# Performance work log

Measured on AMD Instinct MI355X. Metric: run time of the kernel, lower is better.

## Reference

```python
import jax, jax.numpy as jnp
import numpy as np

B, T, C = 4, 2048, 2048
H = 16
D = C // H  # head_dim = 128
THETA = 10000.0


def rope_cos_sin(t, d, dtype=jnp.float32):
    inv_freq = 1.0 / (THETA ** (jnp.arange(0, d, 2, dtype=jnp.float32) / d))  # [D/2]
    pos = jnp.arange(t, dtype=jnp.float32)
    freqs = jnp.outer(pos, inv_freq)                 # [T, D/2]
    emb = jnp.concatenate([freqs, freqs], axis=-1)   # [T, D]
    return jnp.cos(emb).astype(dtype), jnp.sin(emb).astype(dtype)


def rotate_half(x):
    x1, x2 = jnp.split(x, 2, axis=-1)
    return jnp.concatenate([-x2, x1], axis=-1)


def setup_inputs() -> dict:
    key = jax.random.key(0)
    k1, k2, k3 = jax.random.split(key, 3)
    x = jax.random.normal(k1, (B, T, C), dtype=jnp.float32)
    Wqkv = jax.random.normal(k2, (C, 3 * C), dtype=jnp.float32) * (1.0 / np.sqrt(C))
    Wout = jax.random.normal(k3, (C, C), dtype=jnp.float32) * (1.0 / np.sqrt(C))
    return {"x": x, "Wqkv": Wqkv, "Wout": Wout}


def reference(x, Wqkv, Wout):
    b, t, c = x.shape
    qkv = jnp.einsum('btc,cd->btd', x, Wqkv)          # [B,T,3C]
    q, k, v = jnp.split(qkv, 3, axis=-1)
    # [B,T,C] -> [B,H,T,D]
    q = q.reshape(b, t, H, D).transpose(0, 2, 1, 3)
    k = k.reshape(b, t, H, D).transpose(0, 2, 1, 3)
    v = v.reshape(b, t, H, D).transpose(0, 2, 1, 3)
    cos, sin = rope_cos_sin(t, D, x.dtype)            # [T,D]
    cos = cos[None, None]                             # [1,1,T,D]
    sin = sin[None, None]
    q = q * cos + rotate_half(q) * sin
    k = k * cos + rotate_half(k) * sin
    scale = 1.0 / np.sqrt(D)
    scores = jnp.einsum('bhqd,bhkd->bhqk', q, k) * scale
    causal = jnp.tril(jnp.ones((t, t), dtype=bool))
    scores = jnp.where(causal[None, None], scores, jnp.finfo(scores.dtype).min)
    attn = jax.nn.softmax(scores, axis=-1)
    y = jnp.einsum('bhqk,bhkd->bhqd', attn, v)        # [B,H,T,D]
    y = y.transpose(0, 2, 1, 3).reshape(b, t, c)      # [B,T,C]
    return jnp.einsum('btc,cd->btd', y, Wout)
```

## Files before the change

kernel.cpp:

```cpp
#include <hip/hip_runtime.h>
#include <hip/hip_bf16.h>
#include <cmath>

#define Bsz   4
#define Tlen  2048
#define Cdim  2048
#define Hn    16
#define Dh    128
#define N_QKV 6144
#define Mrows 8192

typedef __bf16 bf16x8 __attribute__((ext_vector_type(8)));
typedef __bf16 bf16x4 __attribute__((ext_vector_type(4)));
typedef float  f32x4  __attribute__((ext_vector_type(4)));

__device__ __forceinline__ f32x4 mfma16(bf16x8 a, bf16x8 b, f32x4 c) {
  return __builtin_amdgcn_mfma_f32_16x16x32_bf16(a, b, c, 0, 0, 0);
}

__device__ __forceinline__ void gl16(const void* g, void* l) {
  __builtin_amdgcn_global_load_lds(
      (const __attribute__((address_space(1))) void*)g,
      (__attribute__((address_space(3))) void*)l, 16, 0, 0);
}

__global__ void rope_table_k(float* __restrict__ cosT, float* __restrict__ sinT) {
  int idx = blockIdx.x * 256 + threadIdx.x;
  int t = idx >> 6, i = idx & 63;
  float invf = __expf(-(float)i * 0.14391156698f);
  float a = (float)t * invf;
  float s, c;
  sincosf(a, &s, &c);
  cosT[idx] = c;
  sinT[idx] = s;
}

__global__ __launch_bounds__(256) void f32_to_bf16_k(
    const float* __restrict__ src, __bf16* __restrict__ dst) {
  size_t i = ((size_t)blockIdx.x * 256 + threadIdx.x) * 8;
  f32x4 a = *(const f32x4*)(src + i);
  f32x4 b = *(const f32x4*)(src + i + 4);
  bf16x8 o;
  o[0] = (__bf16)a[0]; o[1] = (__bf16)a[1]; o[2] = (__bf16)a[2]; o[3] = (__bf16)a[3];
  o[4] = (__bf16)b[0]; o[5] = (__bf16)b[1]; o[6] = (__bf16)b[2]; o[7] = (__bf16)b[3];
  *(bf16x8*)(dst + i) = o;
}

__global__ __launch_bounds__(256) void transpose_to_bf16_k(
    const float* __restrict__ src, __bf16* __restrict__ dst, int K, int N) {
  __shared__ float tile[32][33];
  int n0 = blockIdx.x * 32, k0 = blockIdx.y * 32;
  int tr = threadIdx.x >> 3, tc = (threadIdx.x & 7) * 4;
  f32x4 v = *(const f32x4*)&src[(size_t)(k0 + tr) * N + n0 + tc];
  tile[tr][tc + 0] = v[0]; tile[tr][tc + 1] = v[1];
  tile[tr][tc + 2] = v[2]; tile[tr][tc + 3] = v[3];
  __syncthreads();
  bf16x4 w;
  w[0] = (__bf16)tile[tc + 0][tr];
  w[1] = (__bf16)tile[tc + 1][tr];
  w[2] = (__bf16)tile[tc + 2][tr];
  w[3] = (__bf16)tile[tc + 3][tr];
  *(bf16x4*)&dst[(size_t)(n0 + tr) * K + k0 + tc] = w;
}

__global__ __launch_bounds__(512, 2) void qkv_gemm(
    const __bf16* __restrict__ Xb, const __bf16* __restrict__ Wt,
    __bf16* __restrict__ Qo, __bf16* __restrict__ Ko, __bf16* __restrict__ Vo,
    const float* __restrict__ cosT, const float* __restrict__ sinT)
{
  __shared__ union SM {
    struct { __bf16 A[2][256 * 64]; __bf16 B[2][256 * 64]; } s;
    float C[64][265];
  } sm;

  const int tid = threadIdx.x, lane = tid & 63, wid = tid >> 6;
  const int g = lane >> 4, l16 = lane & 15;
  const int wr = wid >> 2, wc = wid & 3;

  const int bid = blockIdx.x;
  const int xcd = bid & 7, idx = bid >> 3;
  const int stl = idx >> 4, pos = idx & 15;
  const int m0 = (xcd * 4 + (pos >> 2)) * 256;
  const int n0 = (stl * 4 + (pos & 3)) * 256;

  const int srow = tid >> 3;
  const int schk = (tid & 7) ^ (srow & 7);
  const __bf16* gA = Xb + (size_t)(m0 + srow) * Cdim + schk * 8;
  const __bf16* gB = Wt + (size_t)(n0 + srow) * Cdim + schk * 8;
  const int ldst = wid * 512;

  f32x4 acc[8][4] = {};
  const int NT = Cdim / 64;

  #pragma unroll
  for (int r = 0; r < 4; ++r) {
    gl16(gA + (size_t)r * 64 * Cdim, &sm.s.A[0][r * 4096 + ldst]);
    gl16(gB + (size_t)r * 64 * Cdim, &sm.s.B[0][r * 4096 + ldst]);
  }
  #pragma unroll
  for (int r = 0; r < 4; ++r) {
    gl16(gA + 64 + (size_t)r * 64 * Cdim, &sm.s.A[1][r * 4096 + ldst]);
    gl16(gB + 64 + (size_t)r * 64 * Cdim, &sm.s.B[1][r * 4096 + ldst]);
  }

  for (int t = 0; t < NT; ++t) {
    const int p = t & 1;
    if (t < NT - 1) asm volatile("s_waitcnt vmcnt(8)" ::: "memory");
    else            asm volatile("s_waitcnt vmcnt(0)" ::: "memory");
    __builtin_amdgcn_s_barrier();
    __builtin_amdgcn_sched_barrier(0);

    #pragma unroll
    for (int kk = 0; kk < 2; ++kk) {
      bf16x8 a[8], b[4];
      const int ch = (((kk << 2) | g) ^ (l16 & 7)) * 8;
      #pragma unroll
      for (int f = 0; f < 8; ++f)
        a[f] = *(const bf16x8*)&sm.s.A[p][(wr * 128 + f * 16 + l16) * 64 + ch];
      #pragma unroll
      for (int n = 0; n < 4; ++n)
        b[n] = *(const bf16x8*)&sm.s.B[p][(wc * 64 + n * 16 + l16) * 64 + ch];
      #pragma unroll
      for (int f = 0; f < 8; ++f)
        #pragma unroll
        for (int n = 0; n < 4; ++n)
          acc[f][n] = mfma16(a[f], b[n], acc[f][n]);
    }

    __builtin_amdgcn_sched_barrier(0);
    asm volatile("s_waitcnt lgkmcnt(0)" ::: "memory");
    __builtin_amdgcn_s_barrier();

    if (t + 2 < NT) {
      const __bf16* pA = gA + (size_t)(t + 2) * 64;
      const __bf16* pB = gB + (size_t)(t + 2) * 64;
      #pragma unroll
      for (int r = 0; r < 4; ++r) {
        gl16(pA + (size_t)r * 64 * Cdim, &sm.s.A[p][r * 4096 + ldst]);
        gl16(pB + (size_t)r * 64 * Cdim, &sm.s.B[p][r * 4096 + ldst]);
      }
    }
  }

  const int sel = n0 >> 11;
  const int h0  = (n0 & 2047) >> 7;
  const int erow = tid >> 3, q = tid & 7;
  const int dlo = (q & 3) * 16;
  const int clo = (q >> 2) * 128 + dlo;
  const int vcol = tid >> 1, vth = tid & 1;

  #pragma unroll
  for (int rh = 0; rh < 4; ++rh) {
    if (wr == (rh >> 1)) {
      const int fb = (rh & 1) * 4;
      #pragma unroll
      for (int f2 = 0; f2 < 4; ++f2)
        #pragma unroll
        for (int n = 0; n < 4; ++n)
          #pragma unroll
          for (int r = 0; r < 4; ++r)
            sm.C[f2 * 16 + g * 4 + r][wc * 64 + n * 16 + l16] = acc[fb + f2][n][r];
    }
    __syncthreads();
    if (sel == 2) {
      const int hh = h0 + (vcol >> 7), d = vcol & 127;
      const int mb = m0 + rh * 64 + vth * 32;
      const int b_ = mb >> 11, tt = mb & 2047;
      __bf16* outp = Vo + (((size_t)(b_ * Hn + hh)) * Dh + d) * Tlen + tt;
      bf16x8 w[4];
      #pragma unroll
      for (int i = 0; i < 32; ++i)
        w[i >> 3][i & 7] = (__bf16)sm.C[vth * 32 + i][vcol];
      #pragma unroll
      for (int k = 0; k < 4; ++k) *(bf16x8*)&outp[k * 8] = w[k];
    } else {
      __bf16* dst = (sel == 0) ? Qo : Ko;
      const int m = m0 + rh * 64 + erow;
      const int b_ = m >> 11, t = m & 2047;
      __bf16* out = dst + (((size_t)(b_ * Hn + h0 + (q >> 2))) * Tlen + t) * Dh + dlo;
      const float* cb = cosT + t * 64 + dlo;
      const float* sb = sinT + t * 64 + dlo;
      bf16x8 o1[2], o2[2];
      #pragma unroll
      for (int i = 0; i < 16; ++i) {
        float v1 = sm.C[erow][clo + i];
        float v2 = sm.C[erow][clo + i + 64];
        float cs = cb[i], sn = sb[i];
        float r1 = v1 * cs - v2 * sn;
        float r2 = v2 * cs + v1 * sn;
        o1[i >> 3][i & 7] = (__bf16)r1;
        o2[i >> 3][i & 7] = (__bf16)r2;
      }
      *(bf16x8*)&out[0]  = o1[0];
      *(bf16x8*)&out[8]  = o1[1];
      *(bf16x8*)&out[64] = o2[0];
      *(bf16x8*)&out[72] = o2[1];
    }
    __syncthreads();
  }
}

__global__ __launch_bounds__(256, 2) void attn_fwd(
    const __bf16* __restrict__ Qg, const __bf16* __restrict__ Kg,
    const __bf16* __restrict__ Vtg, __bf16* __restrict__ Yg)
{
  __shared__ __bf16 Ks[2][64 * 128];
  __shared__ __bf16 Vt[2][128 * 64];
  __shared__ __bf16 Ps[4][16][72];

  const int tid = threadIdx.x, lane = tid & 63, wid = tid >> 6;
  const int g = lane >> 4, l16 = lane & 15;
  const int qt = gridDim.x - 1 - blockIdx.x;
  const int q0 = qt * 64;
  const size_t bh = (size_t)blockIdx.z * Hn + blockIdx.y;
  const __bf16* Kbase = Kg + bh * ((size_t)Tlen * Dh);
  const __bf16* Vbase = Vtg + bh * ((size_t)Dh * Tlen);

  bf16x8 aq[4];
  {
    const __bf16* qrow = Qg + (bh * Tlen + q0 + wid * 16 + l16) * Dh;
    #pragma unroll
    for (int ks = 0; ks < 4; ++ks)
      aq[ks] = *(const bf16x8*)(qrow + ks * 32 + 8 * g);
  }

  float m_r[4], l_r[4];
  #pragma unroll
  for (int r = 0; r < 4; ++r) { m_r[r] = -1e30f; l_r[r] = 0.f; }
  f32x4 o[8] = {};

  const int NKV = qt + 1;

  const int krow = lane >> 4, kchk = lane & 15;
  const int vrow = lane >> 3, vchk = lane & 7;

#define STAGE_KV(kv0_, buf_)                                                    \
  {                                                                             \
    _Pragma("unroll")                                                           \
    for (int rr = 0; rr < 4; ++rr) {                                            \
      const int row = wid * 16 + rr * 4 + krow;                                 \
      const int sc = kchk ^ (row & 7);                                          \
      gl16(Kbase + (size_t)((kv0_) + row) * Dh + sc * 8,                        \
           &Ks[buf_][(wid * 16 + rr * 4) * 128]);                               \
    }                                                                           \
    _Pragma("unroll")                                                           \
    for (int rr = 0; rr < 4; ++rr) {                                            \
      const int row = wid * 32 + rr * 8 + vrow;                                 \
      const int sc = vchk ^ (row & 7);                                          \
      gl16(Vbase + (size_t)row * Tlen + (kv0_) + sc * 8,                        \
           &Vt[buf_][(wid * 32 + rr * 8) * 64]);                                \
    }                                                                           \
  }

  STAGE_KV(0, 0);

  for (int it = 0; it < NKV; ++it) {
    const int p = it & 1;
    if (it + 1 < NKV) {
      STAGE_KV((it + 1) * 64, (it + 1) & 1);
      asm volatile("s_waitcnt vmcnt(8)" ::: "memory");
    } else {
      asm volatile("s_waitcnt vmcnt(0)" ::: "memory");
    }
    __builtin_amdgcn_s_barrier();
    __builtin_amdgcn_sched_barrier(0);

    f32x4 s[4] = {};
    #pragma unroll
    for (int ks = 0; ks < 4; ++ks) {
      const int ch = ((4 * ks + g) ^ (l16 & 7)) * 8;
      #pragma unroll
      for (int nf = 0; nf < 4; ++nf) {
        bf16x8 bk = *(const bf16x8*)&Ks[p][(nf * 16 + l16) * 128 + ch];
        s[nf] = mfma16(aq[ks], bk, s[nf]);
      }
    }

    const float scl = 0.08838834764831845f;
    #pragma unroll
    for (int nf = 0; nf < 4; ++nf)
      #pragma unroll
      for (int r = 0; r < 4; ++r) s[nf][r] *= scl;
    if ((it + 1) * 64 > q0) {
      #pragma unroll
      for (int nf = 0; nf < 4; ++nf) {
        const int col = nf * 16 + l16;
        #pragma unroll
        for (int r = 0; r < 4; ++r)
          if (col > wid * 16 + 4 * g + r) s[nf][r] = -1e30f;
      }
    }

    float mx[4];
    #pragma unroll
    for (int r = 0; r < 4; ++r)
      mx[r] = fmaxf(fmaxf(s[0][r], s[1][r]), fmaxf(s[2][r], s[3][r]));
    #pragma unroll
    for (int off = 1; off < 16; off <<= 1)
      #pragma unroll
      for (int r = 0; r < 4; ++r)
        mx[r] = fmaxf(mx[r], __shfl_xor(mx[r], off, 64));

    int grow = 0;
    #pragma unroll
    for (int r = 0; r < 4; ++r) grow |= (mx[r] > m_r[r]) ? 1 : 0;
    if (__any(grow)) {
      #pragma unroll
      for (int r = 0; r < 4; ++r) {
        const float mn = fmaxf(m_r[r], mx[r]);
        const float al = __expf(m_r[r] - mn);
        m_r[r] = mn;
        l_r[r] *= al;
        #pragma unroll
        for (int n2 = 0; n2 < 8; ++n2) o[n2][r] *= al;
      }
    }

    float rs[4] = {0.f, 0.f, 0.f, 0.f};
    #pragma unroll
    for (int nf = 0; nf < 4; ++nf)
      #pragma unroll
      for (int r = 0; r < 4; ++r) {
        const float pv = __expf(s[nf][r] - m_r[r]);
        s[nf][r] = pv;
        rs[r] += pv;
      }
    #pragma unroll
    for (int off = 1; off < 16; off <<= 1)
      #pragma unroll
      for (int r = 0; r < 4; ++r) rs[r] += __shfl_xor(rs[r], off, 64);
    #pragma unroll
    for (int r = 0; r < 4; ++r) l_r[r] += rs[r];

    #pragma unroll
    for (int nf = 0; nf < 4; ++nf)
      #pragma unroll
      for (int r = 0; r < 4; ++r)
        Ps[wid][4 * g + r][nf * 16 + l16] = (__bf16)s[nf][r];
    asm volatile("s_waitcnt lgkmcnt(0)" ::: "memory");
    __builtin_amdgcn_sched_barrier(0);

    bf16x8 pa0 = *(const bf16x8*)&Ps[wid][l16][8 * g];
    bf16x8 pa1 = *(const bf16x8*)&Ps[wid][l16][32 + 8 * g];
    const int c0 = (g ^ (l16 & 7)) * 8;
    const int c1 = ((4 + g) ^ (l16 & 7)) * 8;
    #pragma unroll
    for (int n2 = 0; n2 < 8; ++n2) {
      bf16x8 vb0 = *(const bf16x8*)&Vt[p][(n2 * 16 + l16) * 64 + c0];
      bf16x8 vb1 = *(const bf16x8*)&Vt[p][(n2 * 16 + l16) * 64 + c1];
      o[n2] = mfma16(pa0, vb0, o[n2]);
      o[n2] = mfma16(pa1, vb1, o[n2]);
    }

    asm volatile("s_waitcnt lgkmcnt(0)" ::: "memory");
    __builtin_amdgcn_sched_barrier(0);
    __builtin_amdgcn_s_barrier();
  }
#undef STAGE_KV

  float inv[4];
  #pragma unroll
  for (int r = 0; r < 4; ++r) inv[r] = 1.0f / l_r[r];
  __bf16* ybase = Yg + ((size_t)(blockIdx.z * Tlen + q0 + wid * 16)) * Cdim
                + blockIdx.y * Dh;
  #pragma unroll
  for (int n2 = 0; n2 < 8; ++n2)
    #pragma unroll
    for (int r = 0; r < 4; ++r)
      ybase[(size_t)(4 * g + r) * Cdim + n2 * 16 + l16] = (__bf16)(o[n2][r] * inv[r]);
}

__global__ __launch_bounds__(512, 2) void out_gemm(
    const __bf16* __restrict__ Yb, const __bf16* __restrict__ Wt,
    float* __restrict__ O)
{
  __shared__ struct { __bf16 A[2][256 * 64]; __bf16 B[2][256 * 64]; } sm;

  const int tid = threadIdx.x, lane = tid & 63, wid = tid >> 6;
  const int g = lane >> 4, l16 = lane & 15;
  const int wr = wid >> 2, wc = wid & 3;

  const int bid = blockIdx.x;
  const int xcd = bid & 7, idx = bid >> 3;
  const int stl = idx >> 4, pos = idx & 15;
  const int m0 = (xcd * 4 + (pos >> 2)) * 256;
  const int n0 = (stl * 4 + (pos & 3)) * 256;

  const int srow = tid >> 3;
  const int schk = (tid & 7) ^ (srow & 7);
  const __bf16* gA = Yb + (size_t)(m0 + srow) * Cdim + schk * 8;
  const __bf16* gB = Wt + (size_t)(n0 + srow) * Cdim + schk * 8;
  const int ldst = wid * 512;

  f32x4 acc[8][4] = {};
  const int NT = Cdim / 64;

  #pragma unroll
  for (int r = 0; r < 4; ++r) {
    gl16(gA + (size_t)r * 64 * Cdim, &sm.A[0][r * 4096 + ldst]);
    gl16(gB + (size_t)r * 64 * Cdim, &sm.B[0][r * 4096 + ldst]);
  }
  #pragma unroll
  for (int r = 0; r < 4; ++r) {
    gl16(gA + 64 + (size_t)r * 64 * Cdim, &sm.A[1][r * 4096 + ldst]);
    gl16(gB + 64 + (size_t)r * 64 * Cdim, &sm.B[1][r * 4096 + ldst]);
  }

  for (int t = 0; t < NT; ++t) {
    const int p = t & 1;
    if (t < NT - 1) asm volatile("s_waitcnt vmcnt(8)" ::: "memory");
    else            asm volatile("s_waitcnt vmcnt(0)" ::: "memory");
    __builtin_amdgcn_s_barrier();
    __builtin_amdgcn_sched_barrier(0);

    #pragma unroll
    for (int kk = 0; kk < 2; ++kk) {
      bf16x8 a[8], b[4];
      const int ch = (((kk << 2) | g) ^ (l16 & 7)) * 8;
      #pragma unroll
      for (int f = 0; f < 8; ++f)
        a[f] = *(const bf16x8*)&sm.A[p][(wr * 128 + f * 16 + l16) * 64 + ch];
      #pragma unroll
      for (int n = 0; n < 4; ++n)
        b[n] = *(const bf16x8*)&sm.B[p][(wc * 64 + n * 16 + l16) * 64 + ch];
      #pragma unroll
      for (int f = 0; f < 8; ++f)
        #pragma unroll
        for (int n = 0; n < 4; ++n)
          acc[f][n] = mfma16(a[f], b[n], acc[f][n]);
    }

    __builtin_amdgcn_sched_barrier(0);
    asm volatile("s_waitcnt lgkmcnt(0)" ::: "memory");
    __builtin_amdgcn_s_barrier();

    if (t + 2 < NT) {
      const __bf16* pA = gA + (size_t)(t + 2) * 64;
      const __bf16* pB = gB + (size_t)(t + 2) * 64;
      #pragma unroll
      for (int r = 0; r < 4; ++r) {
        gl16(pA + (size_t)r * 64 * Cdim, &sm.A[p][r * 4096 + ldst]);
        gl16(pB + (size_t)r * 64 * Cdim, &sm.B[p][r * 4096 + ldst]);
      }
    }
  }

  #pragma unroll
  for (int f = 0; f < 8; ++f)
    #pragma unroll
    for (int n = 0; n < 4; ++n)
      #pragma unroll
      for (int r = 0; r < 4; ++r)
        O[(size_t)(m0 + wr * 128 + f * 16 + g * 4 + r) * Cdim
          + (n0 + wc * 64 + n * 16 + l16)] = acc[f][n][r];
}

extern "C" void kernel_launch(void* const* d_in, const int* in_sizes, int n_in,
                              void* d_out, int out_size, void* d_ws, size_t ws_size,
                              hipStream_t stream) {
  const float* x    = (const float*)d_in[0];
  const float* Wqkv = (const float*)d_in[1];
  const float* Wout = (const float*)d_in[2];
  float* out = (float*)d_out;

  float*  cosT   = (float*)d_ws;
  float*  sinT   = cosT + Tlen * 64;
  __bf16* Xb     = (__bf16*)(sinT + Tlen * 64);
  __bf16* Wqkv_t = Xb + (size_t)Mrows * Cdim;
  __bf16* Wout_t = Wqkv_t + (size_t)N_QKV * Cdim;
  __bf16* Qb     = Wout_t + (size_t)Cdim * Cdim;
  __bf16* Kb     = Qb + (size_t)Bsz * Hn * Tlen * Dh;
  __bf16* Vb     = Kb + (size_t)Bsz * Hn * Tlen * Dh;
  __bf16* Yb     = Xb;

  rope_table_k<<<dim3(512), dim3(256), 0, stream>>>(cosT, sinT);
  f32_to_bf16_k<<<dim3(Mrows * Cdim / (256 * 8)), dim3(256), 0, stream>>>(x, Xb);
  transpose_to_bf16_k<<<dim3(N_QKV / 32, Cdim / 32), dim3(256), 0, stream>>>(
      Wqkv, Wqkv_t, Cdim, N_QKV);
  transpose_to_bf16_k<<<dim3(Cdim / 32, Cdim / 32), dim3(256), 0, stream>>>(
      Wout, Wout_t, Cdim, Cdim);
  qkv_gemm<<<dim3(768), dim3(512), 0, stream>>>(
      Xb, Wqkv_t, Qb, Kb, Vb, cosT, sinT);
  attn_fwd<<<dim3(Tlen / 64, Hn, Bsz), dim3(256), 0, stream>>>(Qb, Kb, Vb, Yb);
  out_gemm<<<dim3(256), dim3(512), 0, stream>>>(Yb, Wout_t, out);
}
```

Before: 732.2 us.

## Transpose attention MFMA operands so each lane owns one query row

Swaps the MFMA operand order in both attention matmuls so the accumulator is transposed and each lane holds a single query row. The row max and row sum then need two cross-lane shuffles instead of four-step reductions over four rows. The softmax folds scale and log2e into an exp2 FMA, applies the causal mask only on the diagonal tile, packs P into 32-bit LDS words, and writes the output as vectorized bf16x4 stores. It also raises wave priority around the MFMA loops with s_setprio. This trades the VALU and shuffle overhead of softmax for new LDS index patterns that could add bank conflicts.

```diff
diff --git a/kernel.cpp b/kernel.cpp
--- a/kernel.cpp
+++ b/kernel.cpp
@@ -13,6 +13,7 @@
 typedef __bf16 bf16x8 __attribute__((ext_vector_type(8)));
 typedef __bf16 bf16x4 __attribute__((ext_vector_type(4)));
 typedef float  f32x4  __attribute__((ext_vector_type(4)));
+typedef uint32_t u32x2 __attribute__((ext_vector_type(2)));
 
 __device__ __forceinline__ f32x4 mfma16(bf16x8 a, bf16x8 b, f32x4 c) {
   return __builtin_amdgcn_mfma_f32_16x16x32_bf16(a, b, c, 0, 0, 0);
@@ -22,6 +23,12 @@
   __builtin_amdgcn_global_load_lds(
       (const __attribute__((address_space(1))) void*)g,
       (__attribute__((address_space(3))) void*)l, 16, 0, 0);
+}
+
+__device__ __forceinline__ uint32_t pack_bf16(float lo, float hi) {
+  union { __bf16 h; unsigned short u; } a, b;
+  a.h = (__bf16)lo; b.h = (__bf16)hi;
+  return (uint32_t)a.u | ((uint32_t)b.u << 16);
 }
 
 __global__ void rope_table_k(float* __restrict__ cosT, float* __restrict__ sinT) {
@@ -206,7 +213,7 @@
 {
   __shared__ __bf16 Ks[2][64 * 128];
   __shared__ __bf16 Vt[2][128 * 64];
-  __shared__ __bf16 Ps[4][16][72];
+  __shared__ uint32_t Ps2[4][16 * 34 + 2];
 
   const int tid = threadIdx.x, lane = tid & 63, wid = tid >> 6;
   const int g = lane >> 4, l16 = lane & 15;
@@ -216,18 +223,19 @@
   const __bf16* Kbase = Kg + bh * ((size_t)Tlen * Dh);
   const __bf16* Vbase = Vtg + bh * ((size_t)Dh * Tlen);
 
+  const int q_glob = q0 + wid * 16 + l16;
+
   bf16x8 aq[4];
   {
-    const __bf16* qrow = Qg + (bh * Tlen + q0 + wid * 16 + l16) * Dh;
+    const __bf16* qrow = Qg + (bh * Tlen + q_glob) * Dh;
     #pragma unroll
     for (int ks = 0; ks < 4; ++ks)
       aq[ks] = *(const bf16x8*)(qrow + ks * 32 + 8 * g);
   }
 
-  float m_r[4], l_r[4];
-  #pragma unroll
-  for (int r = 0; r < 4; ++r) { m_r[r] = -1e30f; l_r[r] = 0.f; }
+  float m_r = -1e30f, l_r = 0.f;
   f32x4 o[8] = {};
+  const float k_e = 0.08838834764831845f * 1.4426950408889634f;
 
   const int NKV = qt + 1;
 
@@ -266,91 +274,87 @@
     __builtin_amdgcn_sched_barrier(0);
 
     f32x4 s[4] = {};
+    __builtin_amdgcn_s_setprio(1);
     #pragma unroll
     for (int ks = 0; ks < 4; ++ks) {
       const int ch = ((4 * ks + g) ^ (l16 & 7)) * 8;
       #pragma unroll
       for (int nf = 0; nf < 4; ++nf) {
         bf16x8 bk = *(const bf16x8*)&Ks[p][(nf * 16 + l16) * 128 + ch];
-        s[nf] = mfma16(aq[ks], bk, s[nf]);
+        s[nf] = mfma16(bk, aq[ks], s[nf]);
       }
     }
-
-    const float scl = 0.08838834764831845f;
-    #pragma unroll
-    for (int nf = 0; nf < 4; ++nf)
-      #pragma unroll
-      for (int r = 0; r < 4; ++r) s[nf][r] *= scl;
-    if ((it + 1) * 64 > q0) {
-      #pragma unroll
-      for (int nf = 0; nf < 4; ++nf) {
-        const int col = nf * 16 + l16;
+    __builtin_amdgcn_s_setprio(0);
+
+    if (it == qt) {
+      const int kvb = it * 64 + 4 * g;
+      #pragma unroll
+      for (int nf = 0; nf < 4; ++nf)
         #pragma unroll
         for (int r = 0; r < 4; ++r)
-          if (col > wid * 16 + 4 * g + r) s[nf][r] = -1e30f;
+          if (kvb + nf * 16 + r > q_glob) s[nf][r] = -1e30f;
+    }
+
+    float mx = s[0][0];
+    #pragma unroll
+    for (int nf = 0; nf < 4; ++nf)
+      #pragma unroll
+      for (int r = 0; r < 4; ++r) mx = fmaxf(mx, s[nf][r]);
+    mx = fmaxf(mx, __shfl_xor(mx, 16, 64));
+    mx = fmaxf(mx, __shfl_xor(mx, 32, 64));
+
+    if (__any(mx > m_r)) {
+      const float mn = fmaxf(m_r, mx);
+      const float al = exp2f((m_r - mn) * k_e);
+      m_r = mn;
+      l_r *= al;
+      #pragma unroll
+      for (int n2 = 0; n2 < 8; ++n2)
+        #pragma unroll
+        for (int r = 0; r < 4; ++r) o[n2][r] *= al;
+    }
+
+    const float mk = -m_r * k_e;
+    float rs = 0.f;
+    #pragma unroll
+    for (int nf = 0; nf < 4; ++nf)
+      #pragma unroll
+      for (int r = 0; r < 4; ++r) {
+        const float pv = exp2f(fmaf(s[nf][r], k_e, mk));
+        s[nf][r] = pv;
+        rs += pv;
       }
-    }
-
-    float mx[4];
-    #pragma unroll
-    for (int r = 0; r < 4; ++r)
-      mx[r] = fmaxf(fmaxf(s[0][r], s[1][r]), fmaxf(s[2][r], s[3][r]));
-    #pragma unroll
-    for (int off = 1; off < 16; off <<= 1)
-      #pragma unroll
-      for (int r = 0; r < 4; ++r)
-        mx[r] = fmaxf(mx[r], __shfl_xor(mx[r], off, 64));
-
-    int grow = 0;
-    #pragma unroll
-    for (int r = 0; r < 4; ++r) grow |= (mx[r] > m_r[r]) ? 1 : 0;
-    if (__any(grow)) {
-      #pragma unroll
-      for (int r = 0; r < 4; ++r) {
-        const float mn = fmaxf(m_r[r], mx[r]);
-        const float al = __expf(m_r[r] - mn);
-        m_r[r] = mn;
-        l_r[r] *= al;
-        #pragma unroll
-        for (int n2 = 0; n2 < 8; ++n2) o[n2][r] *= al;
-      }
-    }
-
-    float rs[4] = {0.f, 0.f, 0.f, 0.f};
-    #pragma unroll
-    for (int nf = 0; nf < 4; ++nf)
-      #pragma unroll
-      for (int r = 0; r < 4; ++r) {
-        const float pv = __expf(s[nf][r] - m_r[r]);
-        s[nf][r] = pv;
-        rs[r] += pv;
-      }
-    #pragma unroll
-    for (int off = 1; off < 16; off <<= 1)
-      #pragma unroll
-      for (int r = 0; r < 4; ++r) rs[r] += __shfl_xor(rs[r], off, 64);
-    #pragma unroll
-    for (int r = 0; r < 4; ++r) l_r[r] += rs[r];
-
-    #pragma unroll
-    for (int nf = 0; nf < 4; ++nf)
-      #pragma unroll
-      for (int r = 0; r < 4; ++r)
-        Ps[wid][4 * g + r][nf * 16 + l16] = (__bf16)s[nf][r];
+    rs += __shfl_xor(rs, 16, 64);
+    rs += __shfl_xor(rs, 32, 64);
+    l_r += rs;
+
+    #pragma unroll
+    for (int nf = 0; nf < 4; ++nf) {
+      u32x2 wv;
+      wv.x = pack_bf16(s[nf][0], s[nf][1]);
+      wv.y = pack_bf16(s[nf][2], s[nf][3]);
+      *(u32x2*)&Ps2[wid][l16 * 34 + nf * 8 + 2 * g] = wv;
+    }
     asm volatile("s_waitcnt lgkmcnt(0)" ::: "memory");
     __builtin_amdgcn_sched_barrier(0);
 
-    bf16x8 pa0 = *(const bf16x8*)&Ps[wid][l16][8 * g];
-    bf16x8 pa1 = *(const bf16x8*)&Ps[wid][l16][32 + 8 * g];
+    union { u32x2 h[2]; bf16x8 v; } pb0, pb1;
+    pb0.h[0] = *(const u32x2*)&Ps2[wid][l16 * 34 + 4 * g];
+    pb0.h[1] = *(const u32x2*)&Ps2[wid][l16 * 34 + 4 * g + 2];
+    pb1.h[0] = *(const u32x2*)&Ps2[wid][l16 * 34 + 16 + 4 * g];
+    pb1.h[1] = *(const u32x2*)&Ps2[wid][l16 * 34 + 16 + 4 * g + 2];
+
     const int c0 = (g ^ (l16 & 7)) * 8;
     const int c1 = ((4 + g) ^ (l16 & 7)) * 8;
+    __builtin_amdgcn_s_setprio(1);
     #pragma unroll
     for (int n2 = 0; n2 < 8; ++n2) {
       bf16x8 vb0 = *(const bf16x8*)&Vt[p][(n2 * 16 + l16) * 64 + c0];
       bf16x8 vb1 = *(const bf16x8*)&Vt[p][(n2 * 16 + l16) * 64 + c1];
-      o[n2] = mfma16(pa0, vb0, o[n2]);
-      o[n2] = mfma16(pa1, vb1, o[n2]);
-    }
+      o[n2] = mfma16(vb0, pb0.v, o[n2]);
+      o[n2] = mfma16(vb1, pb1.v, o[n2]);
+    }
+    __builtin_amdgcn_s_setprio(0);
 
     asm volatile("s_waitcnt lgkmcnt(0)" ::: "memory");
     __builtin_amdgcn_sched_barrier(0);
@@ -358,16 +362,16 @@
   }
 #undef STAGE_KV
 
-  float inv[4];
-  #pragma unroll
-  for (int r = 0; r < 4; ++r) inv[r] = 1.0f / l_r[r];
-  __bf16* ybase = Yg + ((size_t)(blockIdx.z * Tlen + q0 + wid * 16)) * Cdim
-                + blockIdx.y * Dh;
-  #pragma unroll
-  for (int n2 = 0; n2 < 8; ++n2)
-    #pragma unroll
-    for (int r = 0; r < 4; ++r)
-      ybase[(size_t)(4 * g + r) * Cdim + n2 * 16 + l16] = (__bf16)(o[n2][r] * inv[r]);
+  const float inv = 1.0f / l_r;
+  __bf16* yrow = Yg + ((size_t)(blockIdx.z * Tlen + q0 + wid * 16 + l16)) * Cdim
+               + blockIdx.y * Dh;
+  #pragma unroll
+  for (int n2 = 0; n2 < 8; ++n2) {
+    bf16x4 w;
+    #pragma unroll
+    for (int r = 0; r < 4; ++r) w[r] = (__bf16)(o[n2][r] * inv);
+    *(bf16x4*)&yrow[n2 * 16 + 4 * g] = w;
+  }
 }
 
 __global__ __launch_bounds__(512, 2) void out_gemm(
```

Result: faster. 670.0 us (-8.5%).
